# Optimization experiments

Hardware: AMD Instinct MI355X
Metric: run time of the kernel (lower is better)

Reference implementation:

```python
import jax, jax.numpy as jnp
import numpy as np

N, L, C = 32, 2048, 128
DEM = 8


def setup_inputs() -> dict:
    key = jax.random.key(0)
    ks = jax.random.split(key, 8)
    return {
        "inp0": jax.random.normal(ks[0], (N, L, C), jnp.float32),
        "inp1": jax.random.normal(ks[1], (N, L, C), jnp.float32),
        "inp2": jax.random.normal(ks[2], (N, L, C), jnp.float32),
        "dem": jax.random.normal(ks[3], (N, DEM), jnp.float32),
        "W1": jax.random.normal(ks[4], (DEM, 40), jnp.float32) * (1.0 / np.sqrt(DEM)),
        "b1": jnp.zeros((40,), jnp.float32),
        "W2": jax.random.normal(ks[5], (40, 20), jnp.float32) * (1.0 / np.sqrt(40.0)),
        "b2": jnp.zeros((20,), jnp.float32),
    }


def _causal_pools(x):
    # x: [N, L, C]. Left zero-padding of (L-1) + kernel-L pool at stride 1
    # == causal prefix pools (padding zeros participate in max/avg windows).
    Lt = x.shape[1]
    t = jnp.arange(Lt)
    cmax = jax.lax.cummax(x, axis=1)                       # prefix max of real values
    has_pad = (t < Lt - 1)[None, :, None]                  # windows that still contain pad zeros
    p_max = jnp.where(has_pad, jnp.maximum(cmax, 0.0), cmax)

    def combine(a, b):
        av, ai = a
        bv, bi = b
        take_b = bv > av
        return jnp.where(take_b, bv, av), jnp.where(take_b, bi, ai)

    idx0 = jnp.broadcast_to(t[None, :, None], x.shape).astype(jnp.int32)
    _, amax = jax.lax.associative_scan(combine, (x, idx0), axis=1)
    # if a pad zero is the window max, torch's index (shifted by L-1) points to a
    # (negative) pad position: first pad slot of window t maps to t-(L-1)
    pad_idx = (t - (Lt - 1))[None, :, None].astype(jnp.int32)
    p_max_ind = jnp.where(has_pad & (cmax < 0.0), pad_idx, amax)

    csum = jnp.cumsum(x, axis=1)
    p_avg = csum / jnp.asarray(Lt, x.dtype)               # avg_pool1d counts pad zeros -> /L
    cnt = (t + 1).astype(x.dtype)[None, :, None]
    p_sum = csum / cnt                                     # norm_sum: sum normalized by #real steps
    return p_max, p_max_ind, p_avg, p_sum


def reference(inp0, inp1, inp2, dem, W1, b1, W2, b2):
    patient = []
    inds = []
    acts = []
    for x in (inp0, inp1, inp2):
        p_max, p_max_ind, p_avg, p_sum = _causal_pools(x)
        patient.append(jnp.concatenate([p_max, p_avg, p_sum], axis=-1))
        inds.append(p_max_ind)
        acts.append(jax.lax.stop_gradient(p_max))
    d = jax.nn.relu(jax.nn.relu(dem @ W1 + b1) @ W2 + b2)   # [N, 20]
    d = jnp.broadcast_to(d[:, None, :], (d.shape[0], L, d.shape[-1]))
    out = jnp.concatenate(patient + [d], axis=-1)           # [N, L, 3*384 + 20]
    return (out, inds[0], inds[1], inds[2], acts[0], acts[1], acts[2])
```

## Files before the change

### kernel.cpp

```cpp
#include <hip/hip_runtime.h>
#include <float.h>

#define Nn 32
#define Ll 2048
#define Cc 128
#define NTILES 32
#define TILE 64
#define OUTC 1172
#define NLC (Nn * Ll * Cc)
#define OUT_ELEMS ((size_t)Nn * Ll * OUTC)
#define AGG (3 * Nn * NTILES * Cc)

__global__ void k_agg(const float* __restrict__ x0, const float* __restrict__ x1,
                      const float* __restrict__ x2,
                      float* __restrict__ aggMax, int* __restrict__ aggIdx,
                      float* __restrict__ aggSum) {
    int b = blockIdx.x;
    int inp = b >> 10;
    int rem = b & 1023;
    int n = rem >> 5;
    int tile = rem & 31;
    int c = threadIdx.x;
    const float* x = (inp == 0) ? x0 : ((inp == 1) ? x1 : x2);
    int t0 = tile * TILE;
    const float* p = x + ((size_t)n * Ll + t0) * Cc + c;

    float m = -FLT_MAX; int mi = 0; float s = 0.f;
#pragma unroll 4
    for (int t = 0; t < TILE; ++t) {
        float v = p[(size_t)t * Cc];
        s += v;
        if (v > m) { m = v; mi = t0 + t; }
    }
    int o = ((inp * Nn + n) * NTILES + tile) * Cc + c;
    aggMax[o] = m; aggIdx[o] = mi; aggSum[o] = s;
}

__global__ void k_scan_tiles(float* __restrict__ aggMax, int* __restrict__ aggIdx,
                             float* __restrict__ aggSum) {
    int tid = blockIdx.x * blockDim.x + threadIdx.x;
    if (tid >= 3 * Nn * Cc) return;
    int inp = tid / (Nn * Cc);
    int rem = tid - inp * (Nn * Cc);
    int n = rem >> 7;
    int c = rem & 127;
    int base = ((inp * Nn + n) * NTILES) * Cc + c;

    float m = -FLT_MAX; int mi = 0; float s = 0.f;
    for (int j = 0; j < NTILES; ++j) {
        int o = base + j * Cc;
        float am = aggMax[o]; int ai = aggIdx[o]; float as = aggSum[o];
        aggMax[o] = m; aggIdx[o] = mi; aggSum[o] = s;
        if (am > m) { m = am; mi = ai; }
        s += as;
    }
}

__global__ void k_mlp(const float* __restrict__ dem, const float* __restrict__ W1,
                      const float* __restrict__ b1, const float* __restrict__ W2,
                      const float* __restrict__ b2, float* __restrict__ dvals) {
    int n = threadIdx.x;
    if (n >= Nn) return;
    float h[40];
    float de[8];
#pragma unroll
    for (int k = 0; k < 8; ++k) de[k] = dem[n * 8 + k];
#pragma unroll
    for (int j = 0; j < 40; ++j) {
        float s = b1[j];
#pragma unroll
        for (int k = 0; k < 8; ++k) s += de[k] * W1[k * 40 + j];
        h[j] = fmaxf(s, 0.f);
    }
#pragma unroll
    for (int o = 0; o < 20; ++o) {
        float s = b2[o];
#pragma unroll
        for (int j = 0; j < 40; ++j) s += h[j] * W2[j * 20 + o];
        dvals[n * 20 + o] = fmaxf(s, 0.f);
    }
}

__global__ void k_apply(const float* __restrict__ x0, const float* __restrict__ x1,
                        const float* __restrict__ x2,
                        const float* __restrict__ aggMax, const int* __restrict__ aggIdx,
                        const float* __restrict__ aggSum, const float* __restrict__ dvals,
                        float* __restrict__ out) {
    int b = blockIdx.x;
    int inp = b >> 10;
    int rem = b & 1023;
    int n = rem >> 5;
    int tile = rem & 31;
    int c = threadIdx.x;
    const float* x = (inp == 0) ? x0 : ((inp == 1) ? x1 : x2);
    int t0 = tile * TILE;

    int o = ((inp * Nn + n) * NTILES + tile) * Cc + c;
    float m = aggMax[o]; int mi = aggIdx[o]; float s = aggSum[o];

    const float* p = x + ((size_t)n * Ll + t0) * Cc + c;
    float* orow = out + (size_t)n * Ll * OUTC + (size_t)t0 * OUTC + inp * 384 + c;
    float* inds = out + OUT_ELEMS + (size_t)inp * NLC + ((size_t)n * Ll + t0) * Cc + c;
    float* acts = out + OUT_ELEMS + 3 * (size_t)NLC + (size_t)inp * NLC + ((size_t)n * Ll + t0) * Cc + c;

    const float invL = 1.0f / (float)Ll;
#pragma unroll 4
    for (int tl = 0; tl < TILE; ++tl) {
        int t = t0 + tl;
        float v = p[(size_t)tl * Cc];
        s += v;
        if (v > m) { m = v; mi = t; }
        float cmax = m;
        bool haspad = (t < Ll - 1);
        float pmax = haspad ? fmaxf(cmax, 0.f) : cmax;
        int pidx = (haspad && cmax < 0.f) ? (t - (Ll - 1)) : mi;
        float pavg = s * invL;
        float psum = s / (float)(t + 1);

        size_t ro = (size_t)tl * OUTC;
        orow[ro] = pmax;
        orow[ro + 128] = pavg;
        orow[ro + 256] = psum;
        inds[(size_t)tl * Cc] = (float)pidx;
        acts[(size_t)tl * Cc] = pmax;
    }

    if (inp == 0) {
        float* dout = out + (size_t)n * Ll * OUTC + (size_t)t0 * OUTC + 1152;
        for (int idx = c; idx < TILE * 20; idx += 128) {
            int tl = idx / 20;
            int k = idx - tl * 20;
            dout[(size_t)tl * OUTC + k] = dvals[n * 20 + k];
        }
    }
}

extern "C" void kernel_launch(void* const* d_in, const int* in_sizes, int n_in,
                              void* d_out, int out_size, void* d_ws, size_t ws_size,
                              hipStream_t stream) {
    const float* x0  = (const float*)d_in[0];
    const float* x1  = (const float*)d_in[1];
    const float* x2  = (const float*)d_in[2];
    const float* dem = (const float*)d_in[3];
    const float* W1  = (const float*)d_in[4];
    const float* b1  = (const float*)d_in[5];
    const float* W2  = (const float*)d_in[6];
    const float* b2  = (const float*)d_in[7];
    float* out = (float*)d_out;

    char* ws = (char*)d_ws;
    float* aggMax = (float*)ws;
    int*   aggIdx = (int*)(ws + (size_t)AGG * 4);
    float* aggSum = (float*)(ws + 2 * (size_t)AGG * 4);
    float* dvals  = (float*)(ws + 3 * (size_t)AGG * 4);

    k_agg<<<dim3(3 * Nn * NTILES), dim3(Cc), 0, stream>>>(x0, x1, x2, aggMax, aggIdx, aggSum);
    k_scan_tiles<<<dim3(48), dim3(256), 0, stream>>>(aggMax, aggIdx, aggSum);
    k_mlp<<<dim3(1), dim3(64), 0, stream>>>(dem, W1, b1, W2, b2, dvals);
    k_apply<<<dim3(3 * Nn * NTILES), dim3(Cc), 0, stream>>>(x0, x1, x2, aggMax, aggIdx, aggSum, dvals, out);
}
```

Measured before the change: 695.9 us.

## Vectorize aggregate and apply kernels with float4 loads/stores and smaller tiles

Each thread now handles four channels through float4 loads and stores. A 32-lane group covers one (input, batch, tile) unit, and eight units share a 256-thread block. The time tile is halved to 32 steps, which doubles the number of tiles, and the per-step division is replaced by one reciprocal multiply. The aim is wider memory transactions and more parallel work on a bandwidth-bound kernel. In exchange, the serial tile scan is twice as long and the workspace is larger. The reciprocal multiply can differ slightly from true division in the last bit.

```diff
diff --git a/kernel.cpp b/kernel.cpp
--- a/kernel.cpp
+++ b/kernel.cpp
@@ -4,40 +4,50 @@
 #define Nn 32
 #define Ll 2048
 #define Cc 128
-#define NTILES 32
-#define TILE 64
+#define NTILES 64
+#define TILE 32
 #define OUTC 1172
 #define NLC (Nn * Ll * Cc)
 #define OUT_ELEMS ((size_t)Nn * Ll * OUTC)
-#define AGG (3 * Nn * NTILES * Cc)
+#define NUNITS (3 * Nn * NTILES)
+#define AGG (NUNITS * Cc)
 
-__global__ void k_agg(const float* __restrict__ x0, const float* __restrict__ x1,
-                      const float* __restrict__ x2,
-                      float* __restrict__ aggMax, int* __restrict__ aggIdx,
-                      float* __restrict__ aggSum) {
-    int b = blockIdx.x;
-    int inp = b >> 10;
-    int rem = b & 1023;
-    int n = rem >> 5;
-    int tile = rem & 31;
-    int c = threadIdx.x;
+typedef float  f4 __attribute__((ext_vector_type(4)));
+typedef int    i4 __attribute__((ext_vector_type(4)));
+
+__global__ __launch_bounds__(256) void k_agg(
+        const float* __restrict__ x0, const float* __restrict__ x1,
+        const float* __restrict__ x2,
+        f4* __restrict__ aggMax, i4* __restrict__ aggIdx, f4* __restrict__ aggSum) {
+    int unit = blockIdx.x * 8 + (threadIdx.x >> 5);
+    int lane = threadIdx.x & 31;
+    int inp = unit >> 11;
+    int rem = unit & 2047;
+    int n = rem >> 6;
+    int tile = rem & 63;
     const float* x = (inp == 0) ? x0 : ((inp == 1) ? x1 : x2);
     int t0 = tile * TILE;
-    const float* p = x + ((size_t)n * Ll + t0) * Cc + c;
+    const f4* p = (const f4*)(x + ((size_t)n * Ll + t0) * Cc) + lane;
 
-    float m = -FLT_MAX; int mi = 0; float s = 0.f;
+    f4 m = { -FLT_MAX, -FLT_MAX, -FLT_MAX, -FLT_MAX };
+    i4 mi = { 0, 0, 0, 0 };
+    f4 s = { 0.f, 0.f, 0.f, 0.f };
 #pragma unroll 4
-    for (int t = 0; t < TILE; ++t) {
-        float v = p[(size_t)t * Cc];
-        s += v;
-        if (v > m) { m = v; mi = t0 + t; }
+    for (int tl = 0; tl < TILE; ++tl) {
+        f4 v = p[(size_t)tl * (Cc / 4)];
+        int t = t0 + tl;
+#pragma unroll
+        for (int j = 0; j < 4; ++j) {
+            s[j] += v[j];
+            if (v[j] > m[j]) { m[j] = v[j]; mi[j] = t; }
+        }
     }
-    int o = ((inp * Nn + n) * NTILES + tile) * Cc + c;
+    int o = unit * (Cc / 4) + lane;
     aggMax[o] = m; aggIdx[o] = mi; aggSum[o] = s;
 }
 
-__global__ void k_scan_tiles(float* __restrict__ aggMax, int* __restrict__ aggIdx,
-                             float* __restrict__ aggSum) {
+__global__ __launch_bounds__(256) void k_scan_tiles(
+        float* __restrict__ aggMax, int* __restrict__ aggIdx, float* __restrict__ aggSum) {
     int tid = blockIdx.x * blockDim.x + threadIdx.x;
     if (tid >= 3 * Nn * Cc) return;
     int inp = tid / (Nn * Cc);
@@ -81,53 +91,58 @@
     }
 }
 
-__global__ void k_apply(const float* __restrict__ x0, const float* __restrict__ x1,
-                        const float* __restrict__ x2,
-                        const float* __restrict__ aggMax, const int* __restrict__ aggIdx,
-                        const float* __restrict__ aggSum, const float* __restrict__ dvals,
-                        float* __restrict__ out) {
-    int b = blockIdx.x;
-    int inp = b >> 10;
-    int rem = b & 1023;
-    int n = rem >> 5;
-    int tile = rem & 31;
-    int c = threadIdx.x;
+__global__ __launch_bounds__(256) void k_apply(
+        const float* __restrict__ x0, const float* __restrict__ x1,
+        const float* __restrict__ x2,
+        const f4* __restrict__ aggMax, const i4* __restrict__ aggIdx,
+        const f4* __restrict__ aggSum, const float* __restrict__ dvals,
+        float* __restrict__ out) {
+    int unit = blockIdx.x * 8 + (threadIdx.x >> 5);
+    int lane = threadIdx.x & 31;
+    int inp = unit >> 11;
+    int rem = unit & 2047;
+    int n = rem >> 6;
+    int tile = rem & 63;
     const float* x = (inp == 0) ? x0 : ((inp == 1) ? x1 : x2);
     int t0 = tile * TILE;
 
-    int o = ((inp * Nn + n) * NTILES + tile) * Cc + c;
-    float m = aggMax[o]; int mi = aggIdx[o]; float s = aggSum[o];
+    int o = unit * (Cc / 4) + lane;
+    f4 m = aggMax[o]; i4 mi = aggIdx[o]; f4 s = aggSum[o];
 
-    const float* p = x + ((size_t)n * Ll + t0) * Cc + c;
-    float* orow = out + (size_t)n * Ll * OUTC + (size_t)t0 * OUTC + inp * 384 + c;
-    float* inds = out + OUT_ELEMS + (size_t)inp * NLC + ((size_t)n * Ll + t0) * Cc + c;
-    float* acts = out + OUT_ELEMS + 3 * (size_t)NLC + (size_t)inp * NLC + ((size_t)n * Ll + t0) * Cc + c;
+    const f4* p = (const f4*)(x + ((size_t)n * Ll + t0) * Cc) + lane;
+    f4* omax = (f4*)(out + (size_t)n * Ll * OUTC + (size_t)t0 * OUTC + inp * 384) + lane;
+    f4* oind = (f4*)(out + OUT_ELEMS + (size_t)inp * NLC + ((size_t)n * Ll + t0) * Cc) + lane;
+    f4* oact = (f4*)(out + OUT_ELEMS + 3 * (size_t)NLC + (size_t)inp * NLC + ((size_t)n * Ll + t0) * Cc) + lane;
 
     const float invL = 1.0f / (float)Ll;
 #pragma unroll 4
     for (int tl = 0; tl < TILE; ++tl) {
+        f4 v = p[(size_t)tl * (Cc / 4)];
         int t = t0 + tl;
-        float v = p[(size_t)tl * Cc];
-        s += v;
-        if (v > m) { m = v; mi = t; }
-        float cmax = m;
         bool haspad = (t < Ll - 1);
-        float pmax = haspad ? fmaxf(cmax, 0.f) : cmax;
-        int pidx = (haspad && cmax < 0.f) ? (t - (Ll - 1)) : mi;
-        float pavg = s * invL;
-        float psum = s / (float)(t + 1);
-
-        size_t ro = (size_t)tl * OUTC;
-        orow[ro] = pmax;
-        orow[ro + 128] = pavg;
-        orow[ro + 256] = psum;
-        inds[(size_t)tl * Cc] = (float)pidx;
-        acts[(size_t)tl * Cc] = pmax;
+        float rcnt = 1.0f / (float)(t + 1);
+        f4 pmax, pidx, pavg, psum;
+#pragma unroll
+        for (int j = 0; j < 4; ++j) {
+            s[j] += v[j];
+            if (v[j] > m[j]) { m[j] = v[j]; mi[j] = t; }
+            float cmax = m[j];
+            pmax[j] = haspad ? fmaxf(cmax, 0.f) : cmax;
+            pidx[j] = (float)((haspad && cmax < 0.f) ? (t - (Ll - 1)) : mi[j]);
+            pavg[j] = s[j] * invL;
+            psum[j] = s[j] * rcnt;
+        }
+        size_t ro = (size_t)tl * (OUTC / 4);
+        omax[ro]            = pmax;
+        omax[ro + Cc / 4]   = pavg;
+        omax[ro + Cc / 2]   = psum;
+        oind[(size_t)tl * (Cc / 4)] = pidx;
+        oact[(size_t)tl * (Cc / 4)] = pmax;
     }
 
     if (inp == 0) {
         float* dout = out + (size_t)n * Ll * OUTC + (size_t)t0 * OUTC + 1152;
-        for (int idx = c; idx < TILE * 20; idx += 128) {
+        for (int idx = lane; idx < TILE * 20; idx += 32) {
             int tl = idx / 20;
             int k = idx - tl * 20;
             dout[(size_t)tl * OUTC + k] = dvals[n * 20 + k];
@@ -154,8 +169,10 @@
     float* aggSum = (float*)(ws + 2 * (size_t)AGG * 4);
     float* dvals  = (float*)(ws + 3 * (size_t)AGG * 4);
 
-    k_agg<<<dim3(3 * Nn * NTILES), dim3(Cc), 0, stream>>>(x0, x1, x2, aggMax, aggIdx, aggSum);
+    k_agg<<<dim3(NUNITS / 8), dim3(256), 0, stream>>>(x0, x1, x2,
+        (f4*)aggMax, (i4*)aggIdx, (f4*)aggSum);
     k_scan_tiles<<<dim3(48), dim3(256), 0, stream>>>(aggMax, aggIdx, aggSum);
     k_mlp<<<dim3(1), dim3(64), 0, stream>>>(dem, W1, b1, W2, b2, dvals);
-    k_apply<<<dim3(3 * Nn * NTILES), dim3(Cc), 0, stream>>>(x0, x1, x2, aggMax, aggIdx, aggSum, dvals, out);
+    k_apply<<<dim3(NUNITS / 8), dim3(256), 0, stream>>>(x0, x1, x2,
+        (const f4*)aggMax, (const i4*)aggIdx, (const f4*)aggSum, dvals, out);
 }
```

Result: faster. 671.3 us (-3.5%).
